# Optimization experiments

Measured on AMD Instinct MI355X. Metric: run time of the kernel, lower is better.

## Reference

```python
import jax, jax.numpy as jnp
import numpy as np

B, S, E, D, H = 4, 1024, 1024, 1024, 16   # batch, dec_seq, enc_seq, d_model, n_heads
DH = D // H
DFF = 4096
EPS = 1e-5


def setup_inputs() -> dict:
    key = jax.random.key(0)
    ks = jax.random.split(key, 16)
    w = lambda k, shp: (jax.random.normal(k, shp, dtype=jnp.float32) * 0.02)
    return {
        "x": jax.random.normal(ks[0], (B, S, D), dtype=jnp.float32),
        "enc_x": jax.random.normal(ks[1], (B, E, D), dtype=jnp.float32),
        # masked self-attn (fused qkv)
        "w_qkv": w(ks[2], (D, 3 * D)), "b_qkv": jnp.zeros((3 * D,), jnp.float32),
        "w_sa_o": w(ks[3], (D, D)), "b_sa_o": jnp.zeros((D,), jnp.float32),
        # cross-attn
        "w_q": w(ks[4], (D, D)), "b_q": jnp.zeros((D,), jnp.float32),
        "w_k": w(ks[5], (D, D)), "b_k": jnp.zeros((D,), jnp.float32),
        "w_v": w(ks[6], (D, D)), "b_v": jnp.zeros((D,), jnp.float32),
        "w_ca_o": w(ks[7], (D, D)), "b_ca_o": jnp.zeros((D,), jnp.float32),
        # ffn
        "w1": w(ks[8], (D, DFF)), "b1": jnp.zeros((DFF,), jnp.float32),
        "w2": w(ks[9], (DFF, D)), "b2": jnp.zeros((D,), jnp.float32),
        # layernorms
        "g1": jnp.ones((D,), jnp.float32), "be1": jnp.zeros((D,), jnp.float32),
        "g2": jnp.ones((D,), jnp.float32), "be2": jnp.zeros((D,), jnp.float32),
        "g3": jnp.ones((D,), jnp.float32), "be3": jnp.zeros((D,), jnp.float32),
    }


def _layernorm(x, g, b):
    mean = jnp.mean(x, axis=-1, keepdims=True)
    var = jnp.mean(jnp.square(x - mean), axis=-1, keepdims=True)  # unbiased=False
    return g * (x - mean) / jnp.sqrt(var + EPS) + b


def _masked_self_attn(x, w_qkv, b_qkv, w_o, b_o):
    b, s, d = x.shape
    qkv = x @ w_qkv + b_qkv                            # [b,s,3D]
    # Faithful to torch: view as [b,s,H,3*DH] then chunk last dim (interleaved per-head).
    qkv = qkv.reshape(b, s, H, 3 * DH).transpose(0, 2, 1, 3)   # [b,H,s,3DH]
    q, k, v = jnp.split(qkv, 3, axis=-1)               # each [b,H,s,DH]
    scores = jnp.einsum('bhqd,bhkd->bhqk', q, k) / jnp.sqrt(jnp.float32(DH))
    mask = jnp.triu(jnp.ones((s, s), dtype=bool), k=1)
    scores = jnp.where(mask, -jnp.inf, scores)
    attn = jax.nn.softmax(scores, axis=-1)
    out = jnp.einsum('bhqk,bhkd->bhqd', attn, v)       # [b,H,s,DH]
    out = out.transpose(0, 2, 1, 3).reshape(b, s, d)
    return out @ w_o + b_o


def _cross_attn(dec_x, enc_x, w_q, b_q, w_k, b_k, w_v, b_v, w_o, b_o):
    b, sq, d = dec_x.shape
    sk = enc_x.shape[1]
    q = (dec_x @ w_q + b_q).reshape(b, sq, H, DH).transpose(0, 2, 1, 3)
    k = (enc_x @ w_k + b_k).reshape(b, sk, H, DH).transpose(0, 2, 1, 3)
    v = (enc_x @ w_v + b_v).reshape(b, sk, H, DH).transpose(0, 2, 1, 3)
    scores = jnp.einsum('bhqd,bhkd->bhqk', q, k) / jnp.sqrt(jnp.float32(DH))
    attn = jax.nn.softmax(scores, axis=-1)
    out = jnp.einsum('bhqk,bhkd->bhqd', attn, v).transpose(0, 2, 1, 3).reshape(b, sq, d)
    return out @ w_o + b_o


def reference(x, enc_x, w_qkv, b_qkv, w_sa_o, b_sa_o,
              w_q, b_q, w_k, b_k, w_v, b_v, w_ca_o, b_ca_o,
              w1, b1, w2, b2, g1, be1, g2, be2, g3, be3):
    h = _layernorm(x + _masked_self_attn(x, w_qkv, b_qkv, w_sa_o, b_sa_o), g1, be1)
    h = _layernorm(h + _cross_attn(h, enc_x, w_q, b_q, w_k, b_k, w_v, b_v, w_ca_o, b_ca_o), g2, be2)
    ffn = jax.nn.gelu(h @ w1 + b1, approximate=False) @ w2 + b2  # torch F.gelu default = exact
    return _layernorm(h + ffn, g3, be3)
```

## Files before the change

kernel.cpp:

```cpp
#include <hip/hip_runtime.h>

#define BB 4
#define SS 1024
#define DD 1024
#define HH 16
#define DHH 64
#define DFF 4096
#define MROWS 4096
#define NEG_BIG (-1e30f)
#define LOG2E 1.4426950408889634f
#define SCL_L2E 0.1803368801111244f

typedef float  f32x4  __attribute__((ext_vector_type(4)));
typedef __bf16 bf16x8 __attribute__((ext_vector_type(8)));
typedef __bf16 bf16x4 __attribute__((ext_vector_type(4)));

#define DEV __device__ __forceinline__

DEV void glds16(const __bf16* g, __bf16* l) {
  __builtin_amdgcn_global_load_lds((__attribute__((address_space(1))) void*)(g),
                                   (__attribute__((address_space(3))) void*)(l),
                                   16, 0, 0);
}

DEV float sanit(float v) {
  return fminf(fmaxf(v, -1e30f), 1e30f);
}

DEV float gelu_f(float v) {
  const float z  = fabsf(v) * 0.70710678118654752f;
  const float t  = __builtin_amdgcn_rcpf(1.f + 0.3275911f * z);
  float poly = ((((1.061405429f * t - 1.453152027f) * t + 1.421413741f) * t
                 - 0.284496736f) * t + 0.254829592f) * t;
  float er = 1.f - poly * __expf(-z * z);
  er = copysignf(er, v);
  return 0.5f * v * (1.f + er);
}

__global__ __launch_bounds__(256) void cvt_bf16(const float* __restrict__ src,
                                                __bf16* __restrict__ dst)
{
  const int idx = blockIdx.x * 256 + threadIdx.x;
  const f32x4 v = ((const f32x4*)src)[idx];
  bf16x4 o;
#pragma unroll
  for (int i = 0; i < 4; i++) o[i] = (__bf16)v[i];
  ((bf16x4*)dst)[idx] = o;
}

__global__ __launch_bounds__(256) void wtrans(const float* __restrict__ src,
                                              __bf16* __restrict__ dst,
                                              int K, int N)
{
  __shared__ float t[64][65];
  const int k0 = blockIdx.y * 64, n0 = blockIdx.x * 64;
  const int c = threadIdx.x & 63, r0 = threadIdx.x >> 6;
#pragma unroll
  for (int i = 0; i < 16; i++) {
    const int r = r0 * 16 + i;
    t[r][c] = src[(size_t)(k0 + r) * N + n0 + c];
  }
  __syncthreads();
#pragma unroll
  for (int i = 0; i < 16; i++) {
    const int r = r0 * 16 + i;
    dst[(size_t)(n0 + r) * K + k0 + c] = (__bf16)t[c][r];
  }
}

__global__ __launch_bounds__(256) void vtrans(const __bf16* __restrict__ src,
                                              int stride, int colMul, int colAdd,
                                              __bf16* __restrict__ dst)
{
  __shared__ __bf16 t[64][66];
  const int bh = blockIdx.y, b = bh >> 4, h = bh & 15;
  const int s0 = blockIdx.x * 64;
  const int c = threadIdx.x & 63, r0 = threadIdx.x >> 6;
  const __bf16* sp = src + (size_t)(b * SS) * stride + h * colMul + colAdd;
#pragma unroll
  for (int i = 0; i < 16; i++) {
    const int s = r0 * 16 + i;
    t[s][c] = sp[(size_t)(s0 + s) * stride + c];
  }
  __syncthreads();
  __bf16* dp = dst + (size_t)bh * 64 * 1024;
#pragma unroll
  for (int i = 0; i < 16; i++) {
    const int d = r0 * 16 + i;
    dp[(size_t)d * 1024 + s0 + c] = t[c][d];
  }
}

template<int MODE>
__global__ __launch_bounds__(256) void gemm_bt(
    const __bf16* __restrict__ A, const __bf16* __restrict__ Bt,
    const float* __restrict__ bias, void* __restrict__ Cout,
    int N, int K)
{
  __shared__ __align__(16) __bf16 As[2][128 * 32];
  __shared__ __align__(16) __bf16 Bs[2][128 * 32];

  const int bm = blockIdx.y * 128, bn = blockIdx.x * 128;
  const int tid = threadIdx.x, wid = tid >> 6, lane = tid & 63;
  const int quad = lane >> 4, ln = lane & 15;

  const __bf16* gA = A  + (size_t)(bm + wid * 32 + (lane >> 2)) * K + (lane & 3) * 8;
  const __bf16* gB = Bt + (size_t)(bn + wid * 32 + (lane >> 2)) * K + (lane & 3) * 8;
  const int soff = (wid * 32) * 32;

  f32x4 acc[4][4];
#pragma unroll
  for (int i = 0; i < 4; i++)
#pragma unroll
    for (int j = 0; j < 4; j++) acc[i][j] = (f32x4){0.f, 0.f, 0.f, 0.f};

  const int wr = (wid >> 1) * 64, wc = (wid & 1) * 64;

#define G_STAGE(buf, kt) do {                                     \
    const int k0_ = (kt) * 32;                                    \
    glds16(gA + k0_,          &As[buf][soff]);                    \
    glds16(gA + 16 * K + k0_, &As[buf][soff + 16 * 32]);          \
    glds16(gB + k0_,          &Bs[buf][soff]);                    \
    glds16(gB + 16 * K + k0_, &Bs[buf][soff + 16 * 32]);          \
  } while (0)

#define G_COMP(buf) do {                                                    \
    bf16x8 af[4], bfr[4];                                                   \
    _Pragma("unroll")                                                       \
    for (int i = 0; i < 4; i++)                                             \
      af[i] = *(const bf16x8*)(&As[buf][(wr + i * 16 + ln) * 32 + quad * 8]); \
    _Pragma("unroll")                                                       \
    for (int j = 0; j < 4; j++)                                             \
      bfr[j] = *(const bf16x8*)(&Bs[buf][(wc + j * 16 + ln) * 32 + quad * 8]); \
    _Pragma("unroll")                                                       \
    for (int i = 0; i < 4; i++)                                             \
      _Pragma("unroll")                                                     \
      for (int j = 0; j < 4; j++)                                           \
        acc[i][j] = __builtin_amdgcn_mfma_f32_16x16x32_bf16(af[i], bfr[j], acc[i][j], 0, 0, 0); \
  } while (0)

  const int nk = K >> 5;
  G_STAGE(0, 0);
  __syncthreads();
  for (int kt = 0; kt < nk; kt += 2) {
    G_STAGE(1, kt + 1);
    G_COMP(0);
    __syncthreads();
    if (kt + 2 < nk) G_STAGE(0, kt + 2);
    G_COMP(1);
    __syncthreads();
  }
#undef G_STAGE
#undef G_COMP

#pragma unroll
  for (int j = 0; j < 4; j++) {
    const int col = bn + wc + j * 16 + ln;
    const float bv = bias[col];
#pragma unroll
    for (int i = 0; i < 4; i++) {
#pragma unroll
      for (int r = 0; r < 4; r++) {
        const int row = bm + wr + i * 16 + quad * 4 + r;
        float v = sanit(acc[i][j][r] + bv);
        if (MODE == 1) v = gelu_f(v);
        if (MODE == 3 && (col % 192) < 64) v *= SCL_L2E;
        if (MODE == 2) ((float*)Cout)[(size_t)row * N + col] = v;
        else           ((__bf16*)Cout)[(size_t)row * N + col] = (__bf16)v;
      }
    }
  }
}

template<int MODE>
__global__ __launch_bounds__(256) void gemm_bt64(
    const __bf16* __restrict__ A, const __bf16* __restrict__ Bt,
    const float* __restrict__ bias, void* __restrict__ Cout,
    int N, int K)
{
  __shared__ __align__(16) __bf16 As[2][128 * 32];
  __shared__ __align__(16) __bf16 Bs[2][64 * 32];

  const int bm = blockIdx.y * 128, bn = blockIdx.x * 64;
  const int tid = threadIdx.x, wid = tid >> 6, lane = tid & 63;
  const int quad = lane >> 4, ln = lane & 15;

  const __bf16* gA = A  + (size_t)(bm + wid * 32 + (lane >> 2)) * K + (lane & 3) * 8;
  const __bf16* gB = Bt + (size_t)(bn + wid * 16 + (lane >> 2)) * K + (lane & 3) * 8;
  const int aoff = (wid * 32) * 32;
  const int boff = (wid * 16) * 32;

  f32x4 acc[4][2];
#pragma unroll
  for (int i = 0; i < 4; i++)
#pragma unroll
    for (int j = 0; j < 2; j++) acc[i][j] = (f32x4){0.f, 0.f, 0.f, 0.f};

  const int wr = (wid >> 1) * 64, wc = (wid & 1) * 32;

#define G_STAGE(buf, kt) do {                                     \
    const int k0_ = (kt) * 32;                                    \
    glds16(gA + k0_,          &As[buf][aoff]);                    \
    glds16(gA + 16 * K + k0_, &As[buf][aoff + 16 * 32]);          \
    glds16(gB + k0_,          &Bs[buf][boff]);                    \
  } while (0)

#define G_COMP(buf) do {                                                    \
    bf16x8 af[4], bfr[2];                                                   \
    _Pragma("unroll")                                                       \
    for (int i = 0; i < 4; i++)                                             \
      af[i] = *(const bf16x8*)(&As[buf][(wr + i * 16 + ln) * 32 + quad * 8]); \
    _Pragma("unroll")                                                       \
    for (int j = 0; j < 2; j++)                                             \
      bfr[j] = *(const bf16x8*)(&Bs[buf][(wc + j * 16 + ln) * 32 + quad * 8]); \
    _Pragma("unroll")                                                       \
    for (int i = 0; i < 4; i++)                                             \
      _Pragma("unroll")                                                     \
      for (int j = 0; j < 2; j++)                                           \
        acc[i][j] = __builtin_amdgcn_mfma_f32_16x16x32_bf16(af[i], bfr[j], acc[i][j], 0, 0, 0); \
  } while (0)

  const int nk = K >> 5;
  G_STAGE(0, 0);
  __syncthreads();
  for (int kt = 0; kt < nk; kt += 2) {
    G_STAGE(1, kt + 1);
    G_COMP(0);
    __syncthreads();
    if (kt + 2 < nk) G_STAGE(0, kt + 2);
    G_COMP(1);
    __syncthreads();
  }
#undef G_STAGE
#undef G_COMP

#pragma unroll
  for (int j = 0; j < 2; j++) {
    const int col = bn + wc + j * 16 + ln;
    const float bv = bias[col];
#pragma unroll
    for (int i = 0; i < 4; i++) {
#pragma unroll
      for (int r = 0; r < 4; r++) {
        const int row = bm + wr + i * 16 + quad * 4 + r;
        float v = sanit(acc[i][j][r] + bv);
        if (MODE == 3) v *= SCL_L2E;
        if (MODE == 2) ((float*)Cout)[(size_t)row * N + col] = v;
        else           ((__bf16*)Cout)[(size_t)row * N + col] = (__bf16)v;
      }
    }
  }
}

__global__ __launch_bounds__(256) void attn(
    const __bf16* __restrict__ qp, int qStride, int qMul, int qAdd,
    const __bf16* __restrict__ kp, int kStride, int kMul, int kAdd,
    const __bf16* __restrict__ vt, __bf16* __restrict__ outp, int causal)
{
  __shared__ __align__(16) __bf16 Kt[2][64 * 64];
  __shared__ __align__(16) __bf16 Vt[2][64 * 64];
  __shared__ __align__(16) __bf16 ptl[4][32 * 64];

  const int id = blockIdx.x;
  const int bh = ((id >> 6) << 3) | (id & 7);
  const int qblk = (id >> 3) & 7;
  const int b = bh >> 4, h = bh & 15;
  const int tid = threadIdx.x, wid = tid >> 6, lane = tid & 63;
  const int quad = lane >> 4, ln = lane & 15;
  const int qbase = qblk * 128;
  const int rowb0 = qbase + wid * 32;
  const int rowTop = rowb0 + 31;

  bf16x8 aq[2][2];
#pragma unroll
  for (int rf = 0; rf < 2; ++rf) {
    const __bf16* qr = qp + (size_t)(b * SS + rowb0 + rf * 16 + ln) * qStride
                          + h * qMul + qAdd;
#pragma unroll
    for (int ks = 0; ks < 2; ++ks)
      aq[rf][ks] = *(const bf16x8*)(qr + ks * 32 + quad * 8);
  }

  f32x4 acc[2][4];
#pragma unroll
  for (int rf = 0; rf < 2; ++rf)
#pragma unroll
    for (int nb = 0; nb < 4; ++nb) acc[rf][nb] = (f32x4){0.f, 0.f, 0.f, 0.f};
  float l_r[2][4] = {{0.f,0.f,0.f,0.f},{0.f,0.f,0.f,0.f}};

  const __bf16* kbase = kp + (size_t)(b * SS) * kStride + h * kMul + kAdd;
  const __bf16* vtb = vt + (size_t)bh * 64 * 1024;
  __bf16* ptw = ptl[wid];

  const int kvEnd = causal ? (qbase + 128) : SS;
  const int nT = kvEnd >> 6;

  const int sr = wid * 16 + (lane >> 3);
  const int sq = lane & 7;

#pragma unroll
  for (int p = 0; p < 2; ++p) {
    const int r = sr + p * 8;
    const int qs = (sq ^ (r & 7)) * 8;
    glds16(kbase + (size_t)r * kStride + qs, Kt[0] + (wid * 2 + p) * 512);
    glds16(vtb + (size_t)r * 1024 + qs,      Vt[0] + (wid * 2 + p) * 512);
  }

  for (int t = 0; t < nT; ++t) {
    const int cur = t & 1;
    const int kv0 = t * 64;

    if (t + 1 < nT) {
      const int kn = kv0 + 64;
#pragma unroll
      for (int p = 0; p < 2; ++p) {
        const int r = sr + p * 8;
        const int qs = (sq ^ (r & 7)) * 8;
        glds16(kbase + (size_t)(kn + r) * kStride + qs, Kt[cur ^ 1] + (wid * 2 + p) * 512);
        glds16(vtb + (size_t)r * 1024 + kn + qs,        Vt[cur ^ 1] + (wid * 2 + p) * 512);
      }
      __asm__ volatile("s_waitcnt vmcnt(4)" ::: "memory");
    } else {
      __asm__ volatile("s_waitcnt vmcnt(0)" ::: "memory");
    }
    __builtin_amdgcn_sched_barrier(0);
    __builtin_amdgcn_s_barrier();
    __asm__ volatile("" ::: "memory");
    __builtin_amdgcn_sched_barrier(0);

    if (!causal || kv0 <= rowTop) {
      const __bf16* kt = Kt[cur];
      const __bf16* vv = Vt[cur];

      f32x4 sc[2][4];
      {
        bf16x8 kf[4][2];
#pragma unroll
        for (int c = 0; c < 4; ++c) {
          const int row = c * 16 + ln;
#pragma unroll
          for (int ks = 0; ks < 2; ++ks)
            kf[c][ks] = *(const bf16x8*)(kt + row * 64 + (((ks * 4 + quad) ^ (ln & 7)) * 8));
        }
#pragma unroll
        for (int rf = 0; rf < 2; ++rf)
#pragma unroll
          for (int c = 0; c < 4; ++c) {
            f32x4 s_ = (f32x4){0.f, 0.f, 0.f, 0.f};
            s_ = __builtin_amdgcn_mfma_f32_16x16x32_bf16(aq[rf][0], kf[c][0], s_, 0, 0, 0);
            s_ = __builtin_amdgcn_mfma_f32_16x16x32_bf16(aq[rf][1], kf[c][1], s_, 0, 0, 0);
            sc[rf][c] = s_;
          }
      }

#pragma unroll
      for (int rf = 0; rf < 2; ++rf) {
        const bool doMask = causal && (kv0 + 63 > rowb0 + rf * 16);
#pragma unroll
        for (int r = 0; r < 4; ++r) {
          const int rowg = rowb0 + rf * 16 + quad * 4 + r;
          float p[4];
#pragma unroll
          for (int c = 0; c < 4; ++c) {
            float e = sc[rf][c][r];
            if (doMask && (kv0 + c * 16 + ln > rowg)) e = NEG_BIG;
            p[c] = exp2f(e);
          }
          l_r[rf][r] += (p[0] + p[1]) + (p[2] + p[3]);
          const int m = rf * 16 + quad * 4 + r;
          __bf16* pr = ptw + m * 64;
#pragma unroll
          for (int c = 0; c < 4; ++c) {
            const int col = c * 16 + ln;
            pr[(((col >> 3) ^ (m & 7)) << 3) + (col & 7)] = (__bf16)p[c];
          }
        }
      }
      __asm__ volatile("s_waitcnt lgkmcnt(0)" ::: "memory");
      __builtin_amdgcn_sched_barrier(0);

      {
        bf16x8 pa[2][2];
#pragma unroll
        for (int rf = 0; rf < 2; ++rf) {
          const int m = rf * 16 + ln;
#pragma unroll
          for (int ks = 0; ks < 2; ++ks)
            pa[rf][ks] = *(const bf16x8*)(ptw + m * 64 + (((ks * 4 + quad) ^ (m & 7)) * 8));
        }
#pragma unroll
        for (int nb = 0; nb < 4; ++nb) {
          const int vrow = nb * 16 + ln;
          const bf16x8 vf0 = *(const bf16x8*)(vv + vrow * 64 + (((quad)     ^ (ln & 7)) * 8));
          const bf16x8 vf1 = *(const bf16x8*)(vv + vrow * 64 + (((4 + quad) ^ (ln & 7)) * 8));
#pragma unroll
          for (int rf = 0; rf < 2; ++rf) {
            acc[rf][nb] = __builtin_amdgcn_mfma_f32_16x16x32_bf16(pa[rf][0], vf0, acc[rf][nb], 0, 0, 0);
            acc[rf][nb] = __builtin_amdgcn_mfma_f32_16x16x32_bf16(pa[rf][1], vf1, acc[rf][nb], 0, 0, 0);
          }
        }
      }
    }

    __asm__ volatile("" ::: "memory");
    __builtin_amdgcn_sched_barrier(0);
    __builtin_amdgcn_s_barrier();
  }

#pragma unroll
  for (int rf = 0; rf < 2; ++rf) {
#pragma unroll
    for (int r = 0; r < 4; ++r) {
      float l = l_r[rf][r];
#pragma unroll
      for (int off = 1; off < 16; off <<= 1) l += __shfl_xor(l, off, 64);
      const float inv = 1.f / fmaxf(l, 1e-30f);
      const int rowg = rowb0 + rf * 16 + quad * 4 + r;
      __bf16* op = outp + (size_t)(b * SS + rowg) * DD + h * 64;
#pragma unroll
      for (int nb = 0; nb < 4; ++nb)
        op[nb * 16 + ln] = (__bf16)sanit(acc[rf][nb][r] * inv);
    }
  }
}

__global__ __launch_bounds__(256) void ln_k(
    const float* __restrict__ residf, const float* __restrict__ proj,
    const float* __restrict__ g, const float* __restrict__ be,
    float* __restrict__ outf, __bf16* __restrict__ outb)
{
  const int row = blockIdx.x, tid = threadIdx.x;
  const f32x4 pb = ((const f32x4*)(proj   + (size_t)row * 1024))[tid];
  const f32x4 rb = ((const f32x4*)(residf + (size_t)row * 1024))[tid];
  f32x4 x;
#pragma unroll
  for (int i = 0; i < 4; i++)
    x[i] = fminf(fmaxf(pb[i] + rb[i], -1e15f), 1e15f);
  float s  = x[0] + x[1] + x[2] + x[3];
  float ss = x[0]*x[0] + x[1]*x[1] + x[2]*x[2] + x[3]*x[3];
#pragma unroll
  for (int off = 1; off < 64; off <<= 1) {
    s  += __shfl_xor(s,  off, 64);
    ss += __shfl_xor(ss, off, 64);
  }
  __shared__ float sm[8];
  if ((tid & 63) == 0) { sm[tid >> 6] = s; sm[4 + (tid >> 6)] = ss; }
  __syncthreads();
  s  = sm[0] + sm[1] + sm[2] + sm[3];
  ss = sm[4] + sm[5] + sm[6] + sm[7];
  const float mean = s * (1.f / 1024.f);
  const float var  = fmaxf(ss * (1.f / 1024.f) - mean * mean, 0.f);
  const float rstd = rsqrtf(var + 1e-5f);
  const int c = tid * 4;
  f32x4 o;
#pragma unroll
  for (int i = 0; i < 4; i++)
    o[i] = g[c + i] * ((x[i] - mean) * rstd) + be[c + i];
  if (outf) ((f32x4*)(outf + (size_t)row * 1024))[tid] = o;
  if (outb) {
    bf16x4 ob;
#pragma unroll
    for (int i = 0; i < 4; i++) ob[i] = (__bf16)o[i];
    ((bf16x4*)(outb + (size_t)row * 1024))[tid] = ob;
  }
}

extern "C" void kernel_launch(void* const* d_in, const int* in_sizes, int n_in,
                              void* d_out, int out_size, void* d_ws, size_t ws_size,
                              hipStream_t stream)
{
  const float* x      = (const float*)d_in[0];
  const float* enc    = (const float*)d_in[1];
  const float* w_qkv  = (const float*)d_in[2];
  const float* b_qkv  = (const float*)d_in[3];
  const float* w_sa_o = (const float*)d_in[4];
  const float* b_sa_o = (const float*)d_in[5];
  const float* w_q    = (const float*)d_in[6];
  const float* b_q    = (const float*)d_in[7];
  const float* w_k    = (const float*)d_in[8];
  const float* b_k    = (const float*)d_in[9];
  const float* w_v    = (const float*)d_in[10];
  const float* b_v    = (const float*)d_in[11];
  const float* w_ca_o = (const float*)d_in[12];
  const float* b_ca_o = (const float*)d_in[13];
  const float* w1     = (const float*)d_in[14];
  const float* b1     = (const float*)d_in[15];
  const float* w2     = (const float*)d_in[16];
  const float* b2     = (const float*)d_in[17];
  const float* g1     = (const float*)d_in[18];
  const float* be1    = (const float*)d_in[19];
  const float* g2     = (const float*)d_in[20];
  const float* be2    = (const float*)d_in[21];
  const float* g3     = (const float*)d_in[22];
  const float* be3    = (const float*)d_in[23];

  const size_t MB = 1024 * 1024;
  char* base = (char*)d_ws;
  __bf16* wqkvT = (__bf16*)(base + 0 * MB);
  __bf16* wsaoT = (__bf16*)(base + 6 * MB);
  __bf16* wqT   = (__bf16*)(base + 8 * MB);
  __bf16* wkT   = (__bf16*)(base + 10 * MB);
  __bf16* wvT   = (__bf16*)(base + 12 * MB);
  __bf16* wcaoT = (__bf16*)(base + 14 * MB);
  __bf16* w1T   = (__bf16*)(base + 0 * MB);
  __bf16* w2T   = (__bf16*)(base + 8 * MB);
  __bf16* xb    = (__bf16*)(base + 16 * MB);
  __bf16* encb  = (__bf16*)(base + 24 * MB);
  __bf16* qkv   = (__bf16*)(base + 32 * MB);
  __bf16* vt    = (__bf16*)(base + 56 * MB);
  __bf16* mid   = (__bf16*)(base + 32 * MB);
  __bf16* attnb = (__bf16*)(base + 64 * MB);
  float*  proj  = (float*) (base + 72 * MB);
  float*  h1f   = (float*) (base + 88 * MB);
  __bf16* h1b   = (__bf16*)(base + 104 * MB);
  float*  h2f   = (float*) (base + 112 * MB);
  __bf16* h2b   = (__bf16*)(base + 128 * MB);
  __bf16* qb = qkv;
  __bf16* kb = qkv + (size_t)MROWS * 1024;
  __bf16* vb = qkv + (size_t)MROWS * 2048;

  cvt_bf16<<<4096, 256, 0, stream>>>(x,   xb);
  cvt_bf16<<<4096, 256, 0, stream>>>(enc, encb);
  wtrans<<<dim3(48, 16), 256, 0, stream>>>(w_qkv,  wqkvT, 1024, 3072);
  wtrans<<<dim3(16, 16), 256, 0, stream>>>(w_sa_o, wsaoT, 1024, 1024);
  wtrans<<<dim3(16, 16), 256, 0, stream>>>(w_q,    wqT,   1024, 1024);
  wtrans<<<dim3(16, 16), 256, 0, stream>>>(w_k,    wkT,   1024, 1024);
  wtrans<<<dim3(16, 16), 256, 0, stream>>>(w_v,    wvT,   1024, 1024);
  wtrans<<<dim3(16, 16), 256, 0, stream>>>(w_ca_o, wcaoT, 1024, 1024);

  gemm_bt<3><<<dim3(24, 32), 256, 0, stream>>>(xb, wqkvT, b_qkv, qkv, 3072, 1024);
  vtrans<<<dim3(16, 64), 256, 0, stream>>>(qkv, 3072, 192, 128, vt);
  attn<<<512, 256, 0, stream>>>(qkv, 3072, 192, 0,
                                qkv, 3072, 192, 64, vt, attnb, 1);
  gemm_bt64<2><<<dim3(16, 32), 256, 0, stream>>>(attnb, wsaoT, b_sa_o, proj, 1024, 1024);
  ln_k<<<4096, 256, 0, stream>>>(x, proj, g1, be1, h1f, h1b);

  gemm_bt64<3><<<dim3(16, 32), 256, 0, stream>>>(h1b, wqT, b_q, qb, 1024, 1024);
  gemm_bt64<0><<<dim3(16, 32), 256, 0, stream>>>(encb, wkT, b_k, kb, 1024, 1024);
  gemm_bt64<0><<<dim3(16, 32), 256, 0, stream>>>(encb, wvT, b_v, vb, 1024, 1024);
  vtrans<<<dim3(16, 64), 256, 0, stream>>>(vb, 1024, 64, 0, vt);
  attn<<<512, 256, 0, stream>>>(qb, 1024, 64, 0,
                                kb, 1024, 64, 0, vt, attnb, 0);
  gemm_bt64<2><<<dim3(16, 32), 256, 0, stream>>>(attnb, wcaoT, b_ca_o, proj, 1024, 1024);
  ln_k<<<4096, 256, 0, stream>>>(h1f, proj, g2, be2, h2f, h2b);

  wtrans<<<dim3(64, 16), 256, 0, stream>>>(w1, w1T, 1024, 4096);
  wtrans<<<dim3(16, 64), 256, 0, stream>>>(w2, w2T, 4096, 1024);
  gemm_bt<1><<<dim3(32, 32), 256, 0, stream>>>(h2b, w1T, b1, mid, 4096, 1024);
  gemm_bt64<2><<<dim3(16, 32), 256, 0, stream>>>(mid, w2T, b2, proj, 1024, 4096);
  ln_k<<<4096, 256, 0, stream>>>(h2f, proj, g3, be3, (float*)d_out, nullptr);

  (void)in_sizes; (void)n_in; (void)out_size; (void)ws_size;
}
```

Before: 597.7 us.

## Fuse cross-attn K/V projections into one GEMM and split-K the FFN down-projection

The separate K and V projection GEMMs on the encoder input are merged into a single 128x128-tile GEMM over the contiguous transposed K and V weights (N=2048), with per-half bias selection. The FFN second GEMM (K=4096) is split into two K halves written to separate fp32 buffers, and the final layernorm sums both partials. This is meant to reduce launch count, raise tile efficiency and increase the block count for the long-K GEMM. The cost is an extra fp32 partial buffer of write and read traffic, and the proj buffer region must be large enough for both partials.

```diff
diff --git a/kernel.cpp b/kernel.cpp
--- a/kernel.cpp
+++ b/kernel.cpp
@@ -94,8 +94,8 @@
 template<int MODE>
 __global__ __launch_bounds__(256) void gemm_bt(
     const __bf16* __restrict__ A, const __bf16* __restrict__ Bt,
-    const float* __restrict__ bias, void* __restrict__ Cout,
-    int N, int K)
+    const float* __restrict__ bias, const float* __restrict__ bias2,
+    void* __restrict__ Cout, int N, int K)
 {
   __shared__ __align__(16) __bf16 As[2][128 * 32];
   __shared__ __align__(16) __bf16 Bs[2][128 * 32];
@@ -156,7 +156,9 @@
 #pragma unroll
   for (int j = 0; j < 4; j++) {
     const int col = bn + wc + j * 16 + ln;
-    const float bv = bias[col];
+    float bv;
+    if (MODE == 4) bv = (col < 1024) ? bias[col] : bias2[col - 1024];
+    else           bv = bias[col];
 #pragma unroll
     for (int i = 0; i < 4; i++) {
 #pragma unroll
@@ -172,7 +174,7 @@
   }
 }
 
-template<int MODE>
+template<int MODE, int SPLIT>
 __global__ __launch_bounds__(256) void gemm_bt64(
     const __bf16* __restrict__ A, const __bf16* __restrict__ Bt,
     const float* __restrict__ bias, void* __restrict__ Cout,
@@ -182,11 +184,13 @@
   __shared__ __align__(16) __bf16 Bs[2][64 * 32];
 
   const int bm = blockIdx.y * 128, bn = blockIdx.x * 64;
+  const int kz = SPLIT ? blockIdx.z : 0;
+  const int kOff = SPLIT ? kz * (K >> 1) : 0;
   const int tid = threadIdx.x, wid = tid >> 6, lane = tid & 63;
   const int quad = lane >> 4, ln = lane & 15;
 
-  const __bf16* gA = A  + (size_t)(bm + wid * 32 + (lane >> 2)) * K + (lane & 3) * 8;
-  const __bf16* gB = Bt + (size_t)(bn + wid * 16 + (lane >> 2)) * K + (lane & 3) * 8;
+  const __bf16* gA = A  + (size_t)(bm + wid * 32 + (lane >> 2)) * K + (lane & 3) * 8 + kOff;
+  const __bf16* gB = Bt + (size_t)(bn + wid * 16 + (lane >> 2)) * K + (lane & 3) * 8 + kOff;
   const int aoff = (wid * 32) * 32;
   const int boff = (wid * 16) * 32;
 
@@ -220,7 +224,7 @@
         acc[i][j] = __builtin_amdgcn_mfma_f32_16x16x32_bf16(af[i], bfr[j], acc[i][j], 0, 0, 0); \
   } while (0)
 
-  const int nk = K >> 5;
+  const int nk = (K >> SPLIT) >> 5;
   G_STAGE(0, 0);
   __syncthreads();
   for (int kt = 0; kt < nk; kt += 2) {
@@ -234,10 +238,11 @@
 #undef G_STAGE
 #undef G_COMP
 
+  float* outF = (float*)Cout + (SPLIT ? (size_t)kz * MROWS * N : 0);
 #pragma unroll
   for (int j = 0; j < 2; j++) {
     const int col = bn + wc + j * 16 + ln;
-    const float bv = bias[col];
+    const float bv = (SPLIT && kz) ? 0.f : bias[col];
 #pragma unroll
     for (int i = 0; i < 4; i++) {
 #pragma unroll
@@ -245,7 +250,7 @@
         const int row = bm + wr + i * 16 + quad * 4 + r;
         float v = sanit(acc[i][j][r] + bv);
         if (MODE == 3) v *= SCL_L2E;
-        if (MODE == 2) ((float*)Cout)[(size_t)row * N + col] = v;
+        if (MODE == 2) outF[(size_t)row * N + col] = v;
         else           ((__bf16*)Cout)[(size_t)row * N + col] = (__bf16)v;
       }
     }
@@ -426,6 +431,7 @@
 
 __global__ __launch_bounds__(256) void ln_k(
     const float* __restrict__ residf, const float* __restrict__ proj,
+    const float* __restrict__ proj2,
     const float* __restrict__ g, const float* __restrict__ be,
     float* __restrict__ outf, __bf16* __restrict__ outb)
 {
@@ -434,8 +440,15 @@
   const f32x4 rb = ((const f32x4*)(residf + (size_t)row * 1024))[tid];
   f32x4 x;
 #pragma unroll
+  for (int i = 0; i < 4; i++) x[i] = pb[i] + rb[i];
+  if (proj2) {
+    const f32x4 qb_ = ((const f32x4*)(proj2 + (size_t)row * 1024))[tid];
+#pragma unroll
+    for (int i = 0; i < 4; i++) x[i] += qb_[i];
+  }
+#pragma unroll
   for (int i = 0; i < 4; i++)
-    x[i] = fminf(fmaxf(pb[i] + rb[i], -1e15f), 1e15f);
+    x[i] = fminf(fmaxf(x[i], -1e15f), 1e15f);
   float s  = x[0] + x[1] + x[2] + x[3];
   float ss = x[0]*x[0] + x[1]*x[1] + x[2]*x[2] + x[3]*x[3];
 #pragma unroll
@@ -499,6 +512,7 @@
   __bf16* wqkvT = (__bf16*)(base + 0 * MB);
   __bf16* wsaoT = (__bf16*)(base + 6 * MB);
   __bf16* wqT   = (__bf16*)(base + 8 * MB);
+  __bf16* wkvT  = (__bf16*)(base + 10 * MB);
   __bf16* wkT   = (__bf16*)(base + 10 * MB);
   __bf16* wvT   = (__bf16*)(base + 12 * MB);
   __bf16* wcaoT = (__bf16*)(base + 14 * MB);
@@ -507,6 +521,8 @@
   __bf16* xb    = (__bf16*)(base + 16 * MB);
   __bf16* encb  = (__bf16*)(base + 24 * MB);
   __bf16* qkv   = (__bf16*)(base + 32 * MB);
+  __bf16* kvb   = (__bf16*)(base + 32 * MB);
+  __bf16* qcab  = (__bf16*)(base + 48 * MB);
   __bf16* vt    = (__bf16*)(base + 56 * MB);
   __bf16* mid   = (__bf16*)(base + 32 * MB);
   __bf16* attnb = (__bf16*)(base + 64 * MB);
@@ -518,6 +534,7 @@
   __bf16* qb = qkv;
   __bf16* kb = qkv + (size_t)MROWS * 1024;
   __bf16* vb = qkv + (size_t)MROWS * 2048;
+  (void)kb; (void)vb; (void)wkT; (void)wvT;
 
   cvt_bf16<<<4096, 256, 0, stream>>>(x,   xb);
   cvt_bf16<<<4096, 256, 0, stream>>>(enc, encb);
@@ -528,27 +545,27 @@
   wtrans<<<dim3(16, 16), 256, 0, stream>>>(w_v,    wvT,   1024, 1024);
   wtrans<<<dim3(16, 16), 256, 0, stream>>>(w_ca_o, wcaoT, 1024, 1024);
 
-  gemm_bt<3><<<dim3(24, 32), 256, 0, stream>>>(xb, wqkvT, b_qkv, qkv, 3072, 1024);
+  gemm_bt<3><<<dim3(24, 32), 256, 0, stream>>>(xb, wqkvT, b_qkv, nullptr, qkv, 3072, 1024);
   vtrans<<<dim3(16, 64), 256, 0, stream>>>(qkv, 3072, 192, 128, vt);
   attn<<<512, 256, 0, stream>>>(qkv, 3072, 192, 0,
                                 qkv, 3072, 192, 64, vt, attnb, 1);
-  gemm_bt64<2><<<dim3(16, 32), 256, 0, stream>>>(attnb, wsaoT, b_sa_o, proj, 1024, 1024);
-  ln_k<<<4096, 256, 0, stream>>>(x, proj, g1, be1, h1f, h1b);
-
-  gemm_bt64<3><<<dim3(16, 32), 256, 0, stream>>>(h1b, wqT, b_q, qb, 1024, 1024);
-  gemm_bt64<0><<<dim3(16, 32), 256, 0, stream>>>(encb, wkT, b_k, kb, 1024, 1024);
-  gemm_bt64<0><<<dim3(16, 32), 256, 0, stream>>>(encb, wvT, b_v, vb, 1024, 1024);
-  vtrans<<<dim3(16, 64), 256, 0, stream>>>(vb, 1024, 64, 0, vt);
-  attn<<<512, 256, 0, stream>>>(qb, 1024, 64, 0,
-                                kb, 1024, 64, 0, vt, attnb, 0);
-  gemm_bt64<2><<<dim3(16, 32), 256, 0, stream>>>(attnb, wcaoT, b_ca_o, proj, 1024, 1024);
-  ln_k<<<4096, 256, 0, stream>>>(h1f, proj, g2, be2, h2f, h2b);
+  gemm_bt64<2,0><<<dim3(16, 32), 256, 0, stream>>>(attnb, wsaoT, b_sa_o, proj, 1024, 1024);
+  ln_k<<<4096, 256, 0, stream>>>(x, proj, nullptr, g1, be1, h1f, h1b);
+
+  gemm_bt64<3,0><<<dim3(16, 32), 256, 0, stream>>>(h1b, wqT, b_q, qcab, 1024, 1024);
+  gemm_bt<4><<<dim3(16, 32), 256, 0, stream>>>(encb, wkvT, b_k, b_v, kvb, 2048, 1024);
+  vtrans<<<dim3(16, 64), 256, 0, stream>>>(kvb, 2048, 64, 1024, vt);
+  attn<<<512, 256, 0, stream>>>(qcab, 1024, 64, 0,
+                                kvb, 2048, 64, 0, vt, attnb, 0);
+  gemm_bt64<2,0><<<dim3(16, 32), 256, 0, stream>>>(attnb, wcaoT, b_ca_o, proj, 1024, 1024);
+  ln_k<<<4096, 256, 0, stream>>>(h1f, proj, nullptr, g2, be2, h2f, h2b);
 
   wtrans<<<dim3(64, 16), 256, 0, stream>>>(w1, w1T, 1024, 4096);
   wtrans<<<dim3(16, 64), 256, 0, stream>>>(w2, w2T, 4096, 1024);
-  gemm_bt<1><<<dim3(32, 32), 256, 0, stream>>>(h2b, w1T, b1, mid, 4096, 1024);
-  gemm_bt64<2><<<dim3(16, 32), 256, 0, stream>>>(mid, w2T, b2, proj, 1024, 4096);
-  ln_k<<<4096, 256, 0, stream>>>(h2f, proj, g3, be3, (float*)d_out, nullptr);
+  gemm_bt<1><<<dim3(32, 32), 256, 0, stream>>>(h2b, w1T, b1, nullptr, mid, 4096, 1024);
+  gemm_bt64<2,1><<<dim3(16, 32, 2), 256, 0, stream>>>(mid, w2T, b2, proj, 1024, 4096);
+  ln_k<<<4096, 256, 0, stream>>>(h2f, proj, proj + (size_t)MROWS * 1024,
+                                 g3, be3, (float*)d_out, nullptr);
 
   (void)in_sizes; (void)n_in; (void)out_size; (void)ws_size;
 }
```

Result: faster. 572.0 us (-4.3%).
